# Kernel optimization log

Hardware: AMD Instinct MI355X
Metric: run time of the kernel (lower is better)

The kernel has to match this reference:

```python
import jax, jax.numpy as jnp
import numpy as np
import math

B, NG, LS, E = 2, 8, 512, 1024
NH = 16
HD = E // NH
EPS = 1e-6


def rms_norm(x, w):
    xf = x.astype(jnp.float32)
    n = xf * jax.lax.rsqrt(jnp.mean(xf * xf, axis=-1, keepdims=True) + EPS)
    return n.astype(x.dtype) * w


def rotate(x):
    # pairs (a,b) -> (-b, a), matching view(...,-1,2).flip(-1); x[...,0]*=-1
    x2 = x.reshape(*x.shape[:-1], HD // 2, 2)
    out = jnp.stack([-x2[..., 1], x2[..., 0]], axis=-1)
    return out.reshape(x.shape)


def setup_inputs() -> dict:
    key = jax.random.key(0)
    k1, k2, k3 = jax.random.split(key, 3)
    x = jax.random.normal(k1, (B, NG, LS, E), dtype=jnp.float32)
    W_qkv = jax.random.normal(k2, (E, 3 * E), dtype=jnp.float32) * (1.0 / math.sqrt(E))
    ln_w = jnp.ones((E,), dtype=jnp.float32)
    W_proj = jax.random.normal(k3, (E, E), dtype=jnp.float32) * (1.0 / math.sqrt(E))
    return {"x": x, "W_qkv": W_qkv, "ln_w": ln_w, "W_proj": W_proj}


def reference(x, W_qkv, ln_w, W_proj):
    b, ng, ls, _ = x.shape
    qkv = jnp.einsum('bgsc,ce->bgse', x, W_qkv)  # fused QKV projection
    q, k, v = jnp.split(qkv, 3, axis=-1)
    # QK RMSNorm over full embedding dim (before head split)
    q = rms_norm(q, ln_w)
    k = rms_norm(k, ln_w)
    # [B, ng, nh, ls, hd]
    q = q.reshape(b, ng, ls, NH, HD).swapaxes(2, 3)
    k = k.reshape(b, ng, ls, NH, HD).swapaxes(2, 3)
    v = v.reshape(b, ng, ls, NH, HD).swapaxes(2, 3)
    # RoPE (repo's variant: angles duplicated across halves, adjacent-pair rotate)
    pos = 10000.0 ** ((-2.0 * jnp.arange(0, HD, 2, dtype=jnp.float32) - 1.0) / HD)
    token_seq = jnp.arange(ls, dtype=jnp.float32)[:, None] * pos[None, :]  # [ls, hd/2]
    rot = jnp.concatenate([token_seq, token_seq], axis=-1)  # [ls, hd]
    cos, sin = jnp.cos(rot), jnp.sin(rot)
    q = q * cos + rotate(q) * sin
    k = k * cos + rotate(k) * sin
    # causal attention, scale = 1/sqrt(head_dim) (muP=False)
    scale = 1.0 / math.sqrt(HD)
    scores = jnp.einsum('bgnqd,bgnkd->bgnqk', q, k) * scale
    causal = jnp.tril(jnp.ones((ls, ls), dtype=bool))
    scores = jnp.where(causal, scores, jnp.finfo(scores.dtype).min)
    att = jax.nn.softmax(scores, axis=-1)
    y = jnp.einsum('bgnqk,bgnkd->bgnqd', att, v)
    y = y.swapaxes(2, 3).reshape(b, ng, ls, E)
    y = jnp.einsum('bgse,ef->bgsf', y, W_proj)
    return y
```

## Files before the change

kernel.cpp:

```cpp
#include <hip/hip_runtime.h>

typedef unsigned short u16;
typedef unsigned int   u32;
typedef __attribute__((ext_vector_type(8))) short bf16x8;
typedef __attribute__((ext_vector_type(4))) float f32x4;

#define MFMA16(a,b,c) __builtin_amdgcn_mfma_f32_16x16x32_bf16((a),(b),(c),0,0,0)
#define GLD16(gp, lp) __builtin_amdgcn_global_load_lds((const __attribute__((address_space(1))) u32*)(gp), (__attribute__((address_space(3))) u32*)(lp), 16, 0, 0)

#define B_   2
#define NG_  8
#define LS_  512
#define E_   1024
#define NH_  16
#define HD_  64
#define NTOK 8192

__device__ __forceinline__ u16 f2bu(float f){
  u32 u = __builtin_bit_cast(u32, f);
  u32 r = u + 0x7FFFu + ((u >> 16) & 1u);
  return (u16)(r >> 16);
}
__device__ __forceinline__ float b2f(u16 h){
  u32 u = ((u32)h) << 16;
  return __builtin_bit_cast(float, u);
}
__device__ __forceinline__ u32 pk2(float lo, float hi){
  u32 r; asm("v_cvt_pk_bf16_f32 %0, %1, %2" : "=v"(r) : "v"(lo), "v"(hi)); return r;
}

__global__ __launch_bounds__(256) void k_prep(const float* __restrict__ x, u16* __restrict__ xb,
                                              const float* __restrict__ Wqkv, u16* __restrict__ wqkvT,
                                              const float* __restrict__ Wproj, u16* __restrict__ wprojT,
                                              float* __restrict__ ct, float* __restrict__ st){
  int b = blockIdx.x;
  if (b < 8192){
    int i = b * 256 + threadIdx.x;
    float4 v = ((const float4*)x)[i];
    ((ushort4*)xb)[i] = make_ushort4(f2bu(v.x), f2bu(v.y), f2bu(v.z), f2bu(v.w));
    return;
  }
  if (b < 12288){
    const float* W; u16* WT; int Nd, bl;
    if (b < 11264){ W = Wqkv;  WT = wqkvT;  Nd = 3072; bl = b - 8192;  }
    else          { W = Wproj; WT = wprojT; Nd = 1024; bl = b - 11264; }
    int nbx = Nd >> 5;
    int bx = bl % nbx, by = bl / nbx;
    __shared__ float tile[32][33];
    int tx = threadIdx.x & 31, ty = threadIdx.x >> 5;
    int c0 = bx * 32, r0 = by * 32;
    #pragma unroll
    for (int i = 0; i < 4; i++)
      tile[ty + i*8][tx] = W[(size_t)(r0 + ty + i*8) * Nd + c0 + tx];
    __syncthreads();
    #pragma unroll
    for (int i = 0; i < 4; i++)
      WT[(size_t)(c0 + ty + i*8) * 1024 + r0 + tx] = f2bu(tile[tx][ty + i*8]);
    return;
  }
  {
    int i = (b - 12288) * 256 + threadIdx.x;
    int s = i >> 6, d = i & 63, j = d & 31;
    float freq = powf(10000.f, -(4.f * (float)j + 1.f) / 64.f);
    float th = (float)s * freq;
    ct[i] = cosf(th);
    st[i] = sinf(th);
  }
}

template <typename OutT, bool FUSE_VT>
__global__ __launch_bounds__(256, 2) void k_gemm_bt(const u16* __restrict__ A, const u16* __restrict__ Bt,
                                                    OutT* __restrict__ C, u16* __restrict__ vt,
                                                    int M, int N, int K){
  int nbn = N >> 7;
  int cpx = gridDim.x >> 3;
  int bid = (blockIdx.x & 7) * cpx + (blockIdx.x >> 3);
  int tm = bid / nbn, tn = bid % nbn;
  int tid = threadIdx.x;
  int w = tid >> 6, l = tid & 63;
  int lr = l & 15, lg = l >> 4;
  int wm = (w >> 1) * 64, wn = (w & 1) * 64;

  __shared__ u16 smem[2][2][128 * 64];

  const u16* Ab = A  + (size_t)(tm * 128) * K;
  const u16* Bb = Bt + (size_t)(tn * 128) * K;
  int NT = K >> 6;

  int srow0 = tid >> 3, ssl = tid & 7;
  auto stage = [&](int t, int s){
    int k0 = t << 6;
    #pragma unroll
    for (int q = 0; q < 4; q++){
      int row = q * 32 + srow0;
      int sc  = (ssl ^ (row & 7)) << 3;
      GLD16(Ab + (size_t)row * K + k0 + sc, &smem[s][0][q * 2048 + tid * 8]);
    }
    #pragma unroll
    for (int q = 0; q < 4; q++){
      int row = q * 32 + srow0;
      int sc  = (ssl ^ (row & 7)) << 3;
      GLD16(Bb + (size_t)row * K + k0 + sc, &smem[s][1][q * 2048 + tid * 8]);
    }
  };

  f32x4 acc[4][4] = {};

  stage(0, 0);
  stage(1, 1);
  asm volatile("s_waitcnt vmcnt(8)" ::: "memory");
  asm volatile("s_barrier" ::: "memory");

  for (int t = 0; t < NT; t++){
    int s = t & 1;
    const u16* As = smem[s][0];
    const u16* Bs = smem[s][1];
    bf16x8 bfr[4][2], afr[4][2];
    #pragma unroll
    for (int j = 0; j < 4; j++){
      int rb = wn + j * 16 + lr;
      #pragma unroll
      for (int kk = 0; kk < 2; kk++)
        bfr[j][kk] = *(const bf16x8*)&Bs[rb * 64 + ((kk * 32 + lg * 8) ^ ((rb & 7) << 3))];
    }
    #pragma unroll
    for (int i = 0; i < 4; i++){
      int ra = wm + i * 16 + lr;
      #pragma unroll
      for (int kk = 0; kk < 2; kk++)
        afr[i][kk] = *(const bf16x8*)&As[ra * 64 + ((kk * 32 + lg * 8) ^ ((ra & 7) << 3))];
    }
    __builtin_amdgcn_s_setprio(1);
    #pragma unroll
    for (int i = 0; i < 4; i++)
      #pragma unroll
      for (int j = 0; j < 4; j++){
        acc[i][j] = MFMA16(afr[i][0], bfr[j][0], acc[i][j]);
        acc[i][j] = MFMA16(afr[i][1], bfr[j][1], acc[i][j]);
      }
    __builtin_amdgcn_s_setprio(0);
    asm volatile("s_barrier" ::: "memory");
    if (t + 2 < NT){
      stage(t + 2, s);
      asm volatile("s_waitcnt vmcnt(8)" ::: "memory");
      asm volatile("s_barrier" ::: "memory");
    } else if (t + 2 == NT){
      asm volatile("s_waitcnt vmcnt(0)" ::: "memory");
      asm volatile("s_barrier" ::: "memory");
    }
  }

  if constexpr (FUSE_VT){
    if (tn >= 16){
      int h  = (tn - 16) * 2 + (wn >> 6);
      int bg = tm >> 2;
      u16* vbase = vt + (size_t)(bg * 16 + h) * HD_ * LS_;
      #pragma unroll
      for (int i = 0; i < 4; i++){
        int s0 = (tm & 3) * 128 + wm + i * 16 + lg * 4;
        #pragma unroll
        for (int j = 0; j < 4; j++){
          int d = j * 16 + lr;
          ushort4 pk = make_ushort4(f2bu(acc[i][j][0]), f2bu(acc[i][j][1]),
                                    f2bu(acc[i][j][2]), f2bu(acc[i][j][3]));
          *(ushort4*)&vbase[(size_t)d * LS_ + s0] = pk;
        }
      }
      return;
    }
  }

  #pragma unroll
  for (int i = 0; i < 4; i++)
    #pragma unroll
    for (int j = 0; j < 4; j++)
      #pragma unroll
      for (int r = 0; r < 4; r++){
        int row = tm * 128 + wm + i * 16 + lg * 4 + r;
        int col = tn * 128 + wn + j * 16 + lr;
        float v = acc[i][j][r];
        if constexpr (sizeof(OutT) == 2) C[(size_t)row * N + col] = f2bu(v);
        else                             C[(size_t)row * N + col] = v;
      }
}

__global__ __launch_bounds__(256) void k_norm_rope(const u16* __restrict__ qkv, const float* __restrict__ lnw,
                                                   const float* __restrict__ ct, const float* __restrict__ st,
                                                   u16* __restrict__ qh, u16* __restrict__ kh){
  int tok = blockIdx.x;
  int t = threadIdx.x;
  int s = tok & (LS_ - 1);
  int bg = tok >> 9;
  const u16* row = qkv + (size_t)tok * 3072;
  int e0 = t * 4;

  ushort4 q4 = *(const ushort4*)&row[e0];
  ushort4 k4 = *(const ushort4*)&row[1024 + e0];
  float qf[4] = {b2f(q4.x), b2f(q4.y), b2f(q4.z), b2f(q4.w)};
  float kf[4] = {b2f(k4.x), b2f(k4.y), b2f(k4.z), b2f(k4.w)};

  float qss = 0.f, kss = 0.f;
  #pragma unroll
  for (int j = 0; j < 4; j++){ qss += qf[j]*qf[j]; kss += kf[j]*kf[j]; }
  #pragma unroll
  for (int o = 32; o; o >>= 1){ qss += __shfl_down(qss, o); kss += __shfl_down(kss, o); }
  __shared__ float redq[4], redk[4];
  if ((t & 63) == 0){ redq[t >> 6] = qss; redk[t >> 6] = kss; }
  __syncthreads();
  float qsum = redq[0] + redq[1] + redq[2] + redq[3];
  float ksum = redk[0] + redk[1] + redk[2] + redk[3];
  float qr = rsqrtf(qsum * (1.f / 1024.f) + 1e-6f);
  float kr = rsqrtf(ksum * (1.f / 1024.f) + 1e-6f);

  float qn[4], kn[4];
  #pragma unroll
  for (int j = 0; j < 4; j++){
    float wv = lnw[e0 + j];
    qn[j] = qf[j] * qr * wv;
    kn[j] = kf[j] * kr * wv;
  }
  int d0 = e0 & 63, h = e0 >> 6;
  const float* cr = ct + s * 64 + d0;
  const float* sr = st + s * 64 + d0;
  float qo[4], ko[4];
  #pragma unroll
  for (int p = 0; p < 4; p += 2){
    float c0 = cr[p], s0 = sr[p], c1 = cr[p+1], s1 = sr[p+1];
    qo[p]   = qn[p]   * c0 - qn[p+1] * s0;
    qo[p+1] = qn[p+1] * c1 + qn[p]   * s1;
    ko[p]   = kn[p]   * c0 - kn[p+1] * s0;
    ko[p+1] = kn[p+1] * c1 + kn[p]   * s1;
  }
  size_t oidx = (((size_t)bg * NH_ + h) * LS_ + s) * HD_ + d0;
  *(ushort4*)&qh[oidx] = make_ushort4(f2bu(qo[0]*0.125f), f2bu(qo[1]*0.125f), f2bu(qo[2]*0.125f), f2bu(qo[3]*0.125f));
  *(ushort4*)&kh[oidx] = make_ushort4(f2bu(ko[0]), f2bu(ko[1]), f2bu(ko[2]), f2bu(ko[3]));
}

__global__ __launch_bounds__(64) void k_attn(const u16* __restrict__ qh, const u16* __restrict__ kh,
                                             const u16* __restrict__ vt, u16* __restrict__ ytok){
  int bid = blockIdx.x;
  int head = bid & 255;
  int j = 15 - (bid >> 8);
  int l = threadIdx.x & 63;
  int lr = l & 15, lg = l >> 4;
  int q0 = j * 32;
  int ntw = (j >> 1) + 1;

  const u16* Qp = qh + (size_t)head * LS_ * HD_;
  const u16* Kp = kh + (size_t)head * LS_ * HD_;
  const u16* Vp = vt + (size_t)head * HD_ * LS_;
  int bg = head >> 4, h = head & 15;
  u16* Yb = ytok + (size_t)bg * LS_ * E_ + h * HD_;

  bf16x8 aq[2][2];
  #pragma unroll
  for (int mi = 0; mi < 2; mi++)
    #pragma unroll
    for (int kk = 0; kk < 2; kk++)
      aq[mi][kk] = *(const bf16x8*)&Qp[(q0 + mi*16 + lr) * 64 + kk * 32 + lg * 8];

  __shared__ u16 Pw[32 * 72];

  f32x4 o[2][4] = {};
  float mrun[2] = {-1e30f, -1e30f}, lrun[2] = {0.f, 0.f};

  for (int tkv = 0; tkv < ntw; tkv++){
    int kv0 = tkv * 64;
    f32x4 sa[2][4] = {};
    __builtin_amdgcn_s_setprio(1);
    #pragma unroll
    for (int nk = 0; nk < 4; nk++){
      bf16x8 k0 = *(const bf16x8*)&Kp[(kv0 + nk*16 + lr) * 64 + lg * 8];
      bf16x8 k1 = *(const bf16x8*)&Kp[(kv0 + nk*16 + lr) * 64 + 32 + lg * 8];
      #pragma unroll
      for (int mi = 0; mi < 2; mi++){
        sa[mi][nk] = MFMA16(k0, aq[mi][0], sa[mi][nk]);
        sa[mi][nk] = MFMA16(k1, aq[mi][1], sa[mi][nk]);
      }
    }
    __builtin_amdgcn_s_setprio(0);
    if (kv0 + 63 > q0){
      #pragma unroll
      for (int mi = 0; mi < 2; mi++){
        int qg = q0 + mi*16 + lr;
        #pragma unroll
        for (int nk = 0; nk < 4; nk++)
          #pragma unroll
          for (int r = 0; r < 4; r++){
            int kg = kv0 + nk*16 + lg*4 + r;
            if (kg > qg) sa[mi][nk][r] = -1e30f;
          }
      }
    }
    float pmax[2];
    #pragma unroll
    for (int mi = 0; mi < 2; mi++){
      float pm = sa[mi][0][0];
      #pragma unroll
      for (int nk = 0; nk < 4; nk++)
        #pragma unroll
        for (int r = 0; r < 4; r++) pm = fmaxf(pm, sa[mi][nk][r]);
      pm = fmaxf(pm, __shfl_xor(pm, 16));
      pm = fmaxf(pm, __shfl_xor(pm, 32));
      pmax[mi] = pm;
    }
    float dm = fmaxf(pmax[0] - mrun[0], pmax[1] - mrun[1]);
    if (!__all(dm <= 8.f)){
      float alpha[2];
      #pragma unroll
      for (int mi = 0; mi < 2; mi++){
        float mnew = fmaxf(mrun[mi], pmax[mi]);
        alpha[mi] = __expf(mrun[mi] - mnew);
        mrun[mi] = mnew;
        lrun[mi] *= alpha[mi];
      }
      #pragma unroll
      for (int r = 0; r < 4; r++){
        float a0 = __shfl(alpha[0], lg * 4 + r);
        float a1 = __shfl(alpha[1], lg * 4 + r);
        #pragma unroll
        for (int nd = 0; nd < 4; nd++){ o[0][nd][r] *= a0; o[1][nd][r] *= a1; }
      }
    }
    #pragma unroll
    for (int mi = 0; mi < 2; mi++){
      float psum = 0.f;
      #pragma unroll
      for (int nk = 0; nk < 4; nk++)
        #pragma unroll
        for (int r = 0; r < 4; r++){
          float pv = __expf(sa[mi][nk][r] - mrun[mi]);
          sa[mi][nk][r] = pv;
          psum += pv;
        }
      psum += __shfl_xor(psum, 16);
      psum += __shfl_xor(psum, 32);
      lrun[mi] += psum;
    }
    #pragma unroll
    for (int mi = 0; mi < 2; mi++)
      #pragma unroll
      for (int nk = 0; nk < 4; nk++){
        *(u32*)&Pw[(mi*16 + lr) * 72 + nk * 16 + lg * 4]     = pk2(sa[mi][nk][0], sa[mi][nk][1]);
        *(u32*)&Pw[(mi*16 + lr) * 72 + nk * 16 + lg * 4 + 2] = pk2(sa[mi][nk][2], sa[mi][nk][3]);
      }
    bf16x8 pa[2][2];
    #pragma unroll
    for (int mi = 0; mi < 2; mi++){
      pa[mi][0] = *(const bf16x8*)&Pw[(mi*16 + lr) * 72 + lg * 8];
      pa[mi][1] = *(const bf16x8*)&Pw[(mi*16 + lr) * 72 + 32 + lg * 8];
    }
    __builtin_amdgcn_s_setprio(1);
    #pragma unroll
    for (int nd = 0; nd < 4; nd++){
      bf16x8 bv0 = *(const bf16x8*)&Vp[(nd*16 + lr) * 512 + kv0 + lg * 8];
      bf16x8 bv1 = *(const bf16x8*)&Vp[(nd*16 + lr) * 512 + kv0 + 32 + lg * 8];
      #pragma unroll
      for (int mi = 0; mi < 2; mi++){
        o[mi][nd] = MFMA16(pa[mi][0], bv0, o[mi][nd]);
        o[mi][nd] = MFMA16(pa[mi][1], bv1, o[mi][nd]);
      }
    }
    __builtin_amdgcn_s_setprio(0);
  }

  #pragma unroll
  for (int mi = 0; mi < 2; mi++){
    float linv = 1.f / lrun[mi];
    #pragma unroll
    for (int r = 0; r < 4; r++){
      float ir = __shfl(linv, lg * 4 + r);
      int qg = q0 + mi*16 + lg * 4 + r;
      #pragma unroll
      for (int nd = 0; nd < 4; nd++)
        Yb[(size_t)qg * E_ + nd * 16 + lr] = f2bu(o[mi][nd][r] * ir);
    }
  }
}

extern "C" void kernel_launch(void* const* d_in, const int* in_sizes, int n_in,
                              void* d_out, int out_size, void* d_ws, size_t ws_size,
                              hipStream_t stream){
  const float* x     = (const float*)d_in[0];
  const float* Wqkv  = (const float*)d_in[1];
  const float* lnw   = (const float*)d_in[2];
  const float* Wproj = (const float*)d_in[3];
  float* out = (float*)d_out;

  u16* p = (u16*)d_ws;
  u16* xb     = p; p += (size_t)NTOK * E_;
  u16* wqkvT  = p; p += (size_t)3 * E_ * E_;
  u16* wprojT = p; p += (size_t)E_ * E_;
  u16* qkv    = p; p += (size_t)NTOK * 3 * E_;
  u16* qhp    = p; p += (size_t)NTOK * E_;
  u16* khp    = p; p += (size_t)NTOK * E_;
  u16* vtp    = p; p += (size_t)NTOK * E_;
  float* ct = (float*)p;
  float* st = ct + LS_ * HD_;

  k_prep<<<12416, 256, 0, stream>>>(x, xb, Wqkv, wqkvT, Wproj, wprojT, ct, st);
  k_gemm_bt<u16, true><<<64 * 24, 256, 0, stream>>>(xb, wqkvT, qkv, vtp, NTOK, 3 * E_, E_);
  k_norm_rope<<<NTOK, 256, 0, stream>>>(qkv, lnw, ct, st, qhp, khp);
  k_attn<<<4096, 64, 0, stream>>>(qhp, khp, vtp, xb);
  k_gemm_bt<float, false><<<64 * 8, 256, 0, stream>>>(xb, wprojT, out, nullptr, NTOK, E_, E_);
}
```

Before: 152.4 us.

## Widen attention KV tile to 128 and split GEMM A-fragment loads into halves

The attention kernel now handles 128 keys per iteration instead of 64. That halves the number of softmax rescale and reduction rounds and the loop overhead per query block, and the P buffer is written with wider 8-byte stores. In exchange it needs more registers for the score tiles and masks more wasted keys on the diagonal block. The GEMM main loop now loads A fragments in two halves with an extra barrier between them, cutting live fragment registers at the cost of one more synchronisation per k-step.

```diff
diff --git a/kernel.cpp b/kernel.cpp
--- a/kernel.cpp
+++ b/kernel.cpp
@@ -115,7 +115,7 @@
     int s = t & 1;
     const u16* As = smem[s][0];
     const u16* Bs = smem[s][1];
-    bf16x8 bfr[4][2], afr[4][2];
+    bf16x8 bfr[4][2], afr[2][2];
     #pragma unroll
     for (int j = 0; j < 4; j++){
       int rb = wn + j * 16 + lr;
@@ -124,7 +124,7 @@
         bfr[j][kk] = *(const bf16x8*)&Bs[rb * 64 + ((kk * 32 + lg * 8) ^ ((rb & 7) << 3))];
     }
     #pragma unroll
-    for (int i = 0; i < 4; i++){
+    for (int i = 0; i < 2; i++){
       int ra = wm + i * 16 + lr;
       #pragma unroll
       for (int kk = 0; kk < 2; kk++)
@@ -132,11 +132,28 @@
     }
     __builtin_amdgcn_s_setprio(1);
     #pragma unroll
-    for (int i = 0; i < 4; i++)
+    for (int i = 0; i < 2; i++)
       #pragma unroll
       for (int j = 0; j < 4; j++){
         acc[i][j] = MFMA16(afr[i][0], bfr[j][0], acc[i][j]);
         acc[i][j] = MFMA16(afr[i][1], bfr[j][1], acc[i][j]);
+      }
+    __builtin_amdgcn_s_setprio(0);
+    asm volatile("s_barrier" ::: "memory");
+    #pragma unroll
+    for (int i = 0; i < 2; i++){
+      int ra = wm + (i + 2) * 16 + lr;
+      #pragma unroll
+      for (int kk = 0; kk < 2; kk++)
+        afr[i][kk] = *(const bf16x8*)&As[ra * 64 + ((kk * 32 + lg * 8) ^ ((ra & 7) << 3))];
+    }
+    __builtin_amdgcn_s_setprio(1);
+    #pragma unroll
+    for (int i = 0; i < 2; i++)
+      #pragma unroll
+      for (int j = 0; j < 4; j++){
+        acc[i + 2][j] = MFMA16(afr[i][0], bfr[j][0], acc[i + 2][j]);
+        acc[i + 2][j] = MFMA16(afr[i][1], bfr[j][1], acc[i + 2][j]);
       }
     __builtin_amdgcn_s_setprio(0);
     asm volatile("s_barrier" ::: "memory");
@@ -244,7 +261,7 @@
   int l = threadIdx.x & 63;
   int lr = l & 15, lg = l >> 4;
   int q0 = j * 32;
-  int ntw = (j >> 1) + 1;
+  int ntw = (j + 4) >> 2;
 
   const u16* Qp = qh + (size_t)head * LS_ * HD_;
   const u16* Kp = kh + (size_t)head * LS_ * HD_;
@@ -259,17 +276,17 @@
     for (int kk = 0; kk < 2; kk++)
       aq[mi][kk] = *(const bf16x8*)&Qp[(q0 + mi*16 + lr) * 64 + kk * 32 + lg * 8];
 
-  __shared__ u16 Pw[32 * 72];
+  __shared__ u16 Pw[32 * 136];
 
   f32x4 o[2][4] = {};
   float mrun[2] = {-1e30f, -1e30f}, lrun[2] = {0.f, 0.f};
 
   for (int tkv = 0; tkv < ntw; tkv++){
-    int kv0 = tkv * 64;
-    f32x4 sa[2][4] = {};
+    int kv0 = tkv * 128;
+    f32x4 sa[2][8] = {};
     __builtin_amdgcn_s_setprio(1);
     #pragma unroll
-    for (int nk = 0; nk < 4; nk++){
+    for (int nk = 0; nk < 8; nk++){
       bf16x8 k0 = *(const bf16x8*)&Kp[(kv0 + nk*16 + lr) * 64 + lg * 8];
       bf16x8 k1 = *(const bf16x8*)&Kp[(kv0 + nk*16 + lr) * 64 + 32 + lg * 8];
       #pragma unroll
@@ -279,12 +296,12 @@
       }
     }
     __builtin_amdgcn_s_setprio(0);
-    if (kv0 + 63 > q0){
+    if (kv0 + 127 > q0){
       #pragma unroll
       for (int mi = 0; mi < 2; mi++){
         int qg = q0 + mi*16 + lr;
         #pragma unroll
-        for (int nk = 0; nk < 4; nk++)
+        for (int nk = 0; nk < 8; nk++)
           #pragma unroll
           for (int r = 0; r < 4; r++){
             int kg = kv0 + nk*16 + lg*4 + r;
@@ -297,7 +314,7 @@
     for (int mi = 0; mi < 2; mi++){
       float pm = sa[mi][0][0];
       #pragma unroll
-      for (int nk = 0; nk < 4; nk++)
+      for (int nk = 0; nk < 8; nk++)
         #pragma unroll
         for (int r = 0; r < 4; r++) pm = fmaxf(pm, sa[mi][nk][r]);
       pm = fmaxf(pm, __shfl_xor(pm, 16));
@@ -326,7 +343,7 @@
     for (int mi = 0; mi < 2; mi++){
       float psum = 0.f;
       #pragma unroll
-      for (int nk = 0; nk < 4; nk++)
+      for (int nk = 0; nk < 8; nk++)
         #pragma unroll
         for (int r = 0; r < 4; r++){
           float pv = __expf(sa[mi][nk][r] - mrun[mi]);
@@ -340,27 +357,27 @@
     #pragma unroll
     for (int mi = 0; mi < 2; mi++)
       #pragma unroll
-      for (int nk = 0; nk < 4; nk++){
-        *(u32*)&Pw[(mi*16 + lr) * 72 + nk * 16 + lg * 4]     = pk2(sa[mi][nk][0], sa[mi][nk][1]);
-        *(u32*)&Pw[(mi*16 + lr) * 72 + nk * 16 + lg * 4 + 2] = pk2(sa[mi][nk][2], sa[mi][nk][3]);
-      }
-    bf16x8 pa[2][2];
-    #pragma unroll
-    for (int mi = 0; mi < 2; mi++){
-      pa[mi][0] = *(const bf16x8*)&Pw[(mi*16 + lr) * 72 + lg * 8];
-      pa[mi][1] = *(const bf16x8*)&Pw[(mi*16 + lr) * 72 + 32 + lg * 8];
-    }
+      for (int nk = 0; nk < 8; nk++){
+        uint2 d01 = make_uint2(pk2(sa[mi][nk][0], sa[mi][nk][1]),
+                               pk2(sa[mi][nk][2], sa[mi][nk][3]));
+        *(uint2*)&Pw[(mi*16 + lr) * 136 + nk * 16 + lg * 4] = d01;
+      }
+    bf16x8 pa[2][4];
+    #pragma unroll
+    for (int mi = 0; mi < 2; mi++)
+      #pragma unroll
+      for (int kk = 0; kk < 4; kk++)
+        pa[mi][kk] = *(const bf16x8*)&Pw[(mi*16 + lr) * 136 + kk * 32 + lg * 8];
     __builtin_amdgcn_s_setprio(1);
     #pragma unroll
-    for (int nd = 0; nd < 4; nd++){
-      bf16x8 bv0 = *(const bf16x8*)&Vp[(nd*16 + lr) * 512 + kv0 + lg * 8];
-      bf16x8 bv1 = *(const bf16x8*)&Vp[(nd*16 + lr) * 512 + kv0 + 32 + lg * 8];
-      #pragma unroll
-      for (int mi = 0; mi < 2; mi++){
-        o[mi][nd] = MFMA16(pa[mi][0], bv0, o[mi][nd]);
-        o[mi][nd] = MFMA16(pa[mi][1], bv1, o[mi][nd]);
-      }
-    }
+    for (int nd = 0; nd < 4; nd++)
+      #pragma unroll
+      for (int kk = 0; kk < 4; kk++){
+        bf16x8 bv = *(const bf16x8*)&Vp[(nd*16 + lr) * 512 + kv0 + kk * 32 + lg * 8];
+        #pragma unroll
+        for (int mi = 0; mi < 2; mi++)
+          o[mi][nd] = MFMA16(pa[mi][kk], bv, o[mi][nd]);
+      }
     __builtin_amdgcn_s_setprio(0);
   }
 
```

Measured after the change: 157.4 us. 3.3% more time.

## Remap GEMM tiles into per-XCD supertiles and split MFMA loop into halves

Applied to the files above, without the earlier changes.

Block-to-tile mapping now groups 4x6 tile supertiles within each XCD's row range, so blocks sharing an L2 reuse A and B tiles. The inner loop loads only half the A fragments at a time, with an extra barrier between the two MFMA halves. This lowers register pressure and interleaves LDS reads with MFMA across waves. The extra barrier per iteration may add synchronization stalls.

```diff
diff --git a/kernel.cpp b/kernel.cpp
--- a/kernel.cpp
+++ b/kernel.cpp
@@ -74,8 +74,20 @@
                                                     int M, int N, int K){
   int nbn = N >> 7;
   int cpx = gridDim.x >> 3;
-  int bid = (blockIdx.x & 7) * cpx + (blockIdx.x >> 3);
-  int tm = bid / nbn, tn = bid % nbn;
+  int xcd = blockIdx.x & 7;
+  int ii  = blockIdx.x >> 3;
+  int rpx = cpx / nbn;
+  int tm, tn;
+  if ((nbn % 6) == 0 && (rpx & 3) == 0){
+    int st = ii / 24, wi = ii % 24;
+    int srn = rpx >> 2;
+    int sr = st % srn, sc = st / srn;
+    tm = xcd * rpx + sr * 4 + (wi / 6);
+    tn = sc * 6 + (wi % 6);
+  } else {
+    int bid = xcd * cpx + ii;
+    tm = bid / nbn; tn = bid % nbn;
+  }
   int tid = threadIdx.x;
   int w = tid >> 6, l = tid & 63;
   int lr = l & 15, lg = l >> 4;
@@ -93,14 +105,14 @@
     #pragma unroll
     for (int q = 0; q < 4; q++){
       int row = q * 32 + srow0;
-      int sc  = (ssl ^ (row & 7)) << 3;
-      GLD16(Ab + (size_t)row * K + k0 + sc, &smem[s][0][q * 2048 + tid * 8]);
+      int sc2 = (ssl ^ (row & 7)) << 3;
+      GLD16(Ab + (size_t)row * K + k0 + sc2, &smem[s][0][q * 2048 + tid * 8]);
     }
     #pragma unroll
     for (int q = 0; q < 4; q++){
       int row = q * 32 + srow0;
-      int sc  = (ssl ^ (row & 7)) << 3;
-      GLD16(Bb + (size_t)row * K + k0 + sc, &smem[s][1][q * 2048 + tid * 8]);
+      int sc2 = (ssl ^ (row & 7)) << 3;
+      GLD16(Bb + (size_t)row * K + k0 + sc2, &smem[s][1][q * 2048 + tid * 8]);
     }
   };
 
@@ -115,7 +127,7 @@
     int s = t & 1;
     const u16* As = smem[s][0];
     const u16* Bs = smem[s][1];
-    bf16x8 bfr[4][2], afr[4][2];
+    bf16x8 bfr[4][2], afr[2][2];
     #pragma unroll
     for (int j = 0; j < 4; j++){
       int rb = wn + j * 16 + lr;
@@ -124,7 +136,7 @@
         bfr[j][kk] = *(const bf16x8*)&Bs[rb * 64 + ((kk * 32 + lg * 8) ^ ((rb & 7) << 3))];
     }
     #pragma unroll
-    for (int i = 0; i < 4; i++){
+    for (int i = 0; i < 2; i++){
       int ra = wm + i * 16 + lr;
       #pragma unroll
       for (int kk = 0; kk < 2; kk++)
@@ -132,11 +144,28 @@
     }
     __builtin_amdgcn_s_setprio(1);
     #pragma unroll
-    for (int i = 0; i < 4; i++)
+    for (int i = 0; i < 2; i++)
       #pragma unroll
       for (int j = 0; j < 4; j++){
         acc[i][j] = MFMA16(afr[i][0], bfr[j][0], acc[i][j]);
         acc[i][j] = MFMA16(afr[i][1], bfr[j][1], acc[i][j]);
+      }
+    __builtin_amdgcn_s_setprio(0);
+    asm volatile("s_barrier" ::: "memory");
+    #pragma unroll
+    for (int i = 0; i < 2; i++){
+      int ra = wm + (i + 2) * 16 + lr;
+      #pragma unroll
+      for (int kk = 0; kk < 2; kk++)
+        afr[i][kk] = *(const bf16x8*)&As[ra * 64 + ((kk * 32 + lg * 8) ^ ((ra & 7) << 3))];
+    }
+    __builtin_amdgcn_s_setprio(1);
+    #pragma unroll
+    for (int i = 0; i < 2; i++)
+      #pragma unroll
+      for (int j = 0; j < 4; j++){
+        acc[i + 2][j] = MFMA16(afr[i][0], bfr[j][0], acc[i + 2][j]);
+        acc[i + 2][j] = MFMA16(afr[i][1], bfr[j][1], acc[i + 2][j]);
       }
     __builtin_amdgcn_s_setprio(0);
     asm volatile("s_barrier" ::: "memory");
```

Measured after the change: 150.8 us, median of 3. About the same (-1.0%).
